# Kernel tuning notes

Hardware: AMD Instinct MI355X
Metric: run time of the kernel (lower is better)

The kernel has to match this reference:

```python
import jax, jax.numpy as jnp
import numpy as np

N_NODES = 100000
N_EDGES = 1600000
IN_DIM = 256
HID_DIM = 128


def gcn_conv(x, W, b, row, col, norm, n_nodes):
    """PyG-style GCNConv: out[col] += norm * (x @ W)[row], then + bias.

    row/col/norm already include self-loops and symmetric normalization.
    """
    xw = x @ W                                  # [N, D_out]
    msgs = xw[row] * norm[:, None]              # [E', D_out]
    out = jax.ops.segment_sum(msgs, col, num_segments=n_nodes)
    return out + b


def _build_norm(edge_index, n_nodes):
    # add self-loops
    loops = jnp.arange(n_nodes, dtype=edge_index.dtype)
    row = jnp.concatenate([edge_index[0], loops])
    col = jnp.concatenate([edge_index[1], loops])
    # symmetric normalization: deg computed over target (col), as in PyG gcn_norm
    deg = jax.ops.segment_sum(jnp.ones_like(col, dtype=jnp.float32), col,
                              num_segments=n_nodes)
    dinv = jnp.where(deg > 0, jax.lax.rsqrt(deg), 0.0)
    norm = dinv[row] * dinv[col]
    return row, col, norm


def setup_inputs() -> dict:
    key = jax.random.key(0)
    k1, k2, k3, k4 = jax.random.split(key, 4)
    x = jax.random.normal(k1, (N_NODES, IN_DIM), dtype=jnp.float32)
    edge_index = jax.random.randint(k2, (2, N_EDGES), 0, N_NODES, dtype=jnp.int64)
    # Glorot-ish init for weights
    W1 = jax.random.normal(k3, (IN_DIM, HID_DIM), dtype=jnp.float32) / np.sqrt(IN_DIM)
    W2 = jax.random.normal(k4, (HID_DIM, HID_DIM), dtype=jnp.float32) / np.sqrt(HID_DIM)
    b1 = jnp.zeros((HID_DIM,), dtype=jnp.float32)
    b2 = jnp.zeros((HID_DIM,), dtype=jnp.float32)
    return {"x": x, "edge_index": edge_index, "W1": W1, "b1": b1, "W2": W2, "b2": b2}


def reference(x, edge_index, W1, b1, W2, b2):
    n_nodes = x.shape[0]
    row, col, norm = _build_norm(edge_index, n_nodes)
    h = jnp.tanh(gcn_conv(x, W1, b1, row, col, norm, n_nodes))
    h = jnp.tanh(gcn_conv(h, W2, b2, row, col, norm, n_nodes))
    return h
```

## Files before the change

kernel.cpp:

```cpp
#include <hip/hip_runtime.h>
#include <cstdint>
#include <cstddef>

#define N_NODES 100000
#define N_EDGES 1600000
#define HID 128
#define SCAN_BLOCKS ((N_NODES + 255) / 256)

using frag_ab = __attribute__((ext_vector_type(8))) short;
using f32x4   = __attribute__((ext_vector_type(4))) float;

__device__ __forceinline__ unsigned short f2bf(float f) {
    uint32_t u = __builtin_bit_cast(uint32_t, f);
    u += 0x7fffu + ((u >> 16) & 1u);
    return (unsigned short)(u >> 16);
}
__device__ __forceinline__ float bf2f(unsigned short u) {
    uint32_t v = (uint32_t)u << 16;
    return __builtin_bit_cast(float, v);
}

__global__ __launch_bounds__(256) void k_count(const int* __restrict__ col,
                                               int* __restrict__ deg) {
    int e = blockIdx.x * 256 + threadIdx.x;
    if (e < N_EDGES) atomicAdd(&deg[col[e]], 1);
}

__global__ __launch_bounds__(256) void k_dinv(const int* __restrict__ deg,
                                              float* __restrict__ dinv) {
    int i = blockIdx.x * 256 + threadIdx.x;
    if (i < N_NODES) dinv[i] = rsqrtf((float)deg[i] + 1.0f);
}

__global__ __launch_bounds__(256) void k_scan1(const int* __restrict__ deg,
                                               int* __restrict__ cursor,
                                               int* __restrict__ bsum) {
    __shared__ int s[256];
    const int t = threadIdx.x;
    const int i = blockIdx.x * 256 + t;
    int v = (i < N_NODES) ? deg[i] : 0;
    s[t] = v;
    __syncthreads();
#pragma unroll
    for (int d = 1; d < 256; d <<= 1) {
        int a = (t >= d) ? s[t - d] : 0;
        __syncthreads();
        s[t] += a;
        __syncthreads();
    }
    if (i < N_NODES) cursor[i] = s[t] - v;
    if (t == 255) bsum[blockIdx.x] = s[t];
}

__global__ __launch_bounds__(512) void k_scan2(int* __restrict__ bsum, int n) {
    __shared__ int s[512];
    const int t = threadIdx.x;
    int v = (t < n) ? bsum[t] : 0;
    s[t] = v;
    __syncthreads();
#pragma unroll
    for (int d = 1; d < 512; d <<= 1) {
        int a = (t >= d) ? s[t - d] : 0;
        __syncthreads();
        s[t] += a;
        __syncthreads();
    }
    if (t < n) bsum[t] = s[t] - v;
}

__global__ __launch_bounds__(256) void k_scan3(int* __restrict__ cursor,
                                               const int* __restrict__ bsum) {
    const int i = blockIdx.x * 256 + threadIdx.x;
    if (i < N_NODES) cursor[i] += bsum[blockIdx.x];
}

__global__ __launch_bounds__(256) void k_place(const int* __restrict__ row,
                                               const int* __restrict__ col,
                                               const float* __restrict__ dinv,
                                               int* __restrict__ cursor,
                                               int* __restrict__ srow,
                                               float* __restrict__ sdnv) {
    const int e = blockIdx.x * 256 + threadIdx.x;
    if (e >= N_EDGES) return;
    const int r = row[e];
    const int c = col[e];
    const int p = atomicAdd(&cursor[c], 1);
    srow[p] = r;
    sdnv[p] = dinv[r];
}

template <int K>
__global__ __launch_bounds__(256) void k_wt(const float* __restrict__ W,
                                            short* __restrict__ Wt) {
    const int idx = blockIdx.x * 256 + threadIdx.x;
    if (idx >= K * HID) return;
    const int k = idx >> 7;
    const int n = idx & 127;
    Wt[n * K + k] = (short)f2bf(W[idx]);
}

template <int K>
__global__ __launch_bounds__(256) void k_mfma_f32A(const float* __restrict__ A,
                                                   const short* __restrict__ Wt,
                                                   unsigned short* __restrict__ C) {
    const int tid  = threadIdx.x;
    const int w    = tid >> 6;
    const int lane = tid & 63;
    const int l15  = lane & 15;
    const int kg   = lane >> 4;
    const int m0   = blockIdx.x * 128;

    f32x4 acc[2][8];
#pragma unroll
    for (int rb = 0; rb < 2; ++rb)
#pragma unroll
        for (int c = 0; c < 8; ++c)
            acc[rb][c] = (f32x4){0.f, 0.f, 0.f, 0.f};

    for (int k0 = 0; k0 < K; k0 += 32) {
        frag_ab afr[2];
#pragma unroll
        for (int rb = 0; rb < 2; ++rb) {
            int ar = m0 + w * 16 + rb * 64 + l15;
            if (ar >= N_NODES) ar = N_NODES - 1;
            const float4* ap =
                reinterpret_cast<const float4*>(A + (size_t)ar * K + k0 + kg * 8);
            const float4 v0 = ap[0];
            const float4 v1 = ap[1];
            afr[rb][0] = (short)f2bf(v0.x); afr[rb][1] = (short)f2bf(v0.y);
            afr[rb][2] = (short)f2bf(v0.z); afr[rb][3] = (short)f2bf(v0.w);
            afr[rb][4] = (short)f2bf(v1.x); afr[rb][5] = (short)f2bf(v1.y);
            afr[rb][6] = (short)f2bf(v1.z); afr[rb][7] = (short)f2bf(v1.w);
        }
#pragma unroll
        for (int c = 0; c < 8; ++c) {
            const frag_ab bfr = *reinterpret_cast<const frag_ab*>(
                Wt + (size_t)(c * 16 + l15) * K + k0 + kg * 8);
            acc[0][c] = __builtin_amdgcn_mfma_f32_16x16x32_bf16(afr[0], bfr, acc[0][c], 0, 0, 0);
            acc[1][c] = __builtin_amdgcn_mfma_f32_16x16x32_bf16(afr[1], bfr, acc[1][c], 0, 0, 0);
        }
    }
#pragma unroll
    for (int rb = 0; rb < 2; ++rb) {
        const int rbase = m0 + w * 16 + rb * 64 + kg * 4;
#pragma unroll
        for (int c = 0; c < 8; ++c)
#pragma unroll
            for (int i = 0; i < 4; ++i) {
                const int rr = rbase + i;
                if (rr < N_NODES) C[(size_t)rr * HID + c * 16 + l15] = f2bf(acc[rb][c][i]);
            }
    }
}

template <int K>
__global__ __launch_bounds__(256) void k_mfma_bf16A(const unsigned short* __restrict__ A,
                                                    const short* __restrict__ Wt,
                                                    unsigned short* __restrict__ C) {
    const int tid  = threadIdx.x;
    const int w    = tid >> 6;
    const int lane = tid & 63;
    const int l15  = lane & 15;
    const int kg   = lane >> 4;
    const int m0   = blockIdx.x * 128;

    f32x4 acc[2][8];
#pragma unroll
    for (int rb = 0; rb < 2; ++rb)
#pragma unroll
        for (int c = 0; c < 8; ++c)
            acc[rb][c] = (f32x4){0.f, 0.f, 0.f, 0.f};

    for (int k0 = 0; k0 < K; k0 += 32) {
        frag_ab afr[2];
#pragma unroll
        for (int rb = 0; rb < 2; ++rb) {
            int ar = m0 + w * 16 + rb * 64 + l15;
            if (ar >= N_NODES) ar = N_NODES - 1;
            afr[rb] = *reinterpret_cast<const frag_ab*>(A + (size_t)ar * K + k0 + kg * 8);
        }
#pragma unroll
        for (int c = 0; c < 8; ++c) {
            const frag_ab bfr = *reinterpret_cast<const frag_ab*>(
                Wt + (size_t)(c * 16 + l15) * K + k0 + kg * 8);
            acc[0][c] = __builtin_amdgcn_mfma_f32_16x16x32_bf16(afr[0], bfr, acc[0][c], 0, 0, 0);
            acc[1][c] = __builtin_amdgcn_mfma_f32_16x16x32_bf16(afr[1], bfr, acc[1][c], 0, 0, 0);
        }
    }
#pragma unroll
    for (int rb = 0; rb < 2; ++rb) {
        const int rbase = m0 + w * 16 + rb * 64 + kg * 4;
#pragma unroll
        for (int c = 0; c < 8; ++c)
#pragma unroll
            for (int i = 0; i < 4; ++i) {
                const int rr = rbase + i;
                if (rr < N_NODES) C[(size_t)rr * HID + c * 16 + l15] = f2bf(acc[rb][c][i]);
            }
    }
}

template <bool OUT_BF16>
__global__ __launch_bounds__(256) void k_gather_act(const unsigned short* __restrict__ xw,
                                                    const int* __restrict__ srow,
                                                    const float* __restrict__ sdnv,
                                                    const int* __restrict__ cursor,
                                                    const float* __restrict__ dinv,
                                                    const float* __restrict__ b,
                                                    void* __restrict__ outv) {
    const int tid = threadIdx.x;
    const int node = blockIdx.x * 8 + (tid >> 5);
    if (node >= N_NODES) return;
    const int ch = (tid & 31) * 4;

    const int start = (node == 0) ? 0 : cursor[node - 1];
    const int end = cursor[node];

    float4 acc = make_float4(0.f, 0.f, 0.f, 0.f);
#pragma unroll 2
    for (int j = start; j < end; ++j) {
        const int r = srow[j];
        const float w = sdnv[j];
        const ushort4 v = *reinterpret_cast<const ushort4*>(xw + (size_t)r * HID + ch);
        acc.x += w * bf2f(v.x);
        acc.y += w * bf2f(v.y);
        acc.z += w * bf2f(v.z);
        acc.w += w * bf2f(v.w);
    }

    const float dc = dinv[node];
    const float s = dc * dc;
    const ushort4 xv = *reinterpret_cast<const ushort4*>(xw + (size_t)node * HID + ch);
    const float4 bv = *reinterpret_cast<const float4*>(b + ch);
    float o0 = tanhf(dc * acc.x + s * bf2f(xv.x) + bv.x);
    float o1 = tanhf(dc * acc.y + s * bf2f(xv.y) + bv.y);
    float o2 = tanhf(dc * acc.z + s * bf2f(xv.z) + bv.z);
    float o3 = tanhf(dc * acc.w + s * bf2f(xv.w) + bv.w);

    if (OUT_BF16) {
        ushort4 o = {f2bf(o0), f2bf(o1), f2bf(o2), f2bf(o3)};
        *reinterpret_cast<ushort4*>((unsigned short*)outv + (size_t)node * HID + ch) = o;
    } else {
        *reinterpret_cast<float4*>((float*)outv + (size_t)node * HID + ch) =
            make_float4(o0, o1, o2, o3);
    }
}

extern "C" void kernel_launch(void* const* d_in, const int* in_sizes, int n_in,
                              void* d_out, int out_size, void* d_ws, size_t ws_size,
                              hipStream_t stream) {
    const float* x  = (const float*)d_in[0];
    const int*   ei = (const int*)d_in[1];
    const int*   row = ei;
    const int*   col = ei + N_EDGES;
    const float* W1 = (const float*)d_in[2];
    const float* b1 = (const float*)d_in[3];
    const float* W2 = (const float*)d_in[4];
    const float* b2 = (const float*)d_in[5];
    float* out = (float*)d_out;

    unsigned short* xwb = (unsigned short*)d_ws;
    unsigned short* h1b = xwb + (size_t)N_NODES * HID;
    float* dinv   = (float*)(h1b + (size_t)N_NODES * HID);
    int*   deg    = (int*)(dinv + N_NODES);
    int*   cursor = deg + N_NODES;
    int*   bsum   = cursor + N_NODES;
    int*   srow   = bsum + 512;
    float* sdnv   = (float*)(srow + N_EDGES);
    short* wt1    = (short*)(sdnv + N_EDGES);
    short* wt2    = wt1 + 128 * 256;

    k_wt<256><<<(256 * HID + 255) / 256, 256, 0, stream>>>(W1, wt1);
    k_wt<128><<<(128 * HID + 255) / 256, 256, 0, stream>>>(W2, wt2);

    hipMemsetAsync(deg, 0, N_NODES * sizeof(int), stream);
    k_count<<<(N_EDGES + 255) / 256, 256, 0, stream>>>(col, deg);
    k_dinv<<<(N_NODES + 255) / 256, 256, 0, stream>>>(deg, dinv);
    k_scan1<<<SCAN_BLOCKS, 256, 0, stream>>>(deg, cursor, bsum);
    k_scan2<<<1, 512, 0, stream>>>(bsum, SCAN_BLOCKS);
    k_scan3<<<SCAN_BLOCKS, 256, 0, stream>>>(cursor, bsum);
    k_place<<<(N_EDGES + 255) / 256, 256, 0, stream>>>(row, col, dinv, cursor, srow, sdnv);

    k_mfma_f32A<256><<<(N_NODES + 127) / 128, 256, 0, stream>>>(x, wt1, xwb);
    k_gather_act<true><<<N_NODES / 8, 256, 0, stream>>>(xwb, srow, sdnv, cursor, dinv, b1, h1b);

    k_mfma_bf16A<128><<<(N_NODES + 127) / 128, 256, 0, stream>>>(h1b, wt2, xwb);
    k_gather_act<false><<<N_NODES / 8, 256, 0, stream>>>(xwb, srow, sdnv, cursor, dinv, b2, out);
}
```

Baseline: 558.3 us.

## Fold source-node dinv scaling into GEMM epilogue and drop per-edge weight array

```diff
diff --git a/kernel.cpp b/kernel.cpp
--- a/kernel.cpp
+++ b/kernel.cpp
@@ -76,17 +76,14 @@
 
 __global__ __launch_bounds__(256) void k_place(const int* __restrict__ row,
                                                const int* __restrict__ col,
-                                               const float* __restrict__ dinv,
                                                int* __restrict__ cursor,
-                                               int* __restrict__ srow,
-                                               float* __restrict__ sdnv) {
+                                               int* __restrict__ srow) {
     const int e = blockIdx.x * 256 + threadIdx.x;
     if (e >= N_EDGES) return;
     const int r = row[e];
     const int c = col[e];
     const int p = atomicAdd(&cursor[c], 1);
     srow[p] = r;
-    sdnv[p] = dinv[r];
 }
 
 template <int K>
@@ -102,6 +99,7 @@
 template <int K>
 __global__ __launch_bounds__(256) void k_mfma_f32A(const float* __restrict__ A,
                                                    const short* __restrict__ Wt,
+                                                   const float* __restrict__ dinv,
                                                    unsigned short* __restrict__ C) {
     const int tid  = threadIdx.x;
     const int w    = tid >> 6;
@@ -143,12 +141,17 @@
 #pragma unroll
     for (int rb = 0; rb < 2; ++rb) {
         const int rbase = m0 + w * 16 + rb * 64 + kg * 4;
+        float dv[4];
+#pragma unroll
+        for (int i = 0; i < 4; ++i)
+            dv[i] = (rbase + i < N_NODES) ? dinv[rbase + i] : 0.f;
 #pragma unroll
         for (int c = 0; c < 8; ++c)
 #pragma unroll
             for (int i = 0; i < 4; ++i) {
                 const int rr = rbase + i;
-                if (rr < N_NODES) C[(size_t)rr * HID + c * 16 + l15] = f2bf(acc[rb][c][i]);
+                if (rr < N_NODES)
+                    C[(size_t)rr * HID + c * 16 + l15] = f2bf(dv[i] * acc[rb][c][i]);
             }
     }
 }
@@ -156,6 +159,7 @@
 template <int K>
 __global__ __launch_bounds__(256) void k_mfma_bf16A(const unsigned short* __restrict__ A,
                                                     const short* __restrict__ Wt,
+                                                    const float* __restrict__ dinv,
                                                     unsigned short* __restrict__ C) {
     const int tid  = threadIdx.x;
     const int w    = tid >> 6;
@@ -190,20 +194,24 @@
 #pragma unroll
     for (int rb = 0; rb < 2; ++rb) {
         const int rbase = m0 + w * 16 + rb * 64 + kg * 4;
+        float dv[4];
+#pragma unroll
+        for (int i = 0; i < 4; ++i)
+            dv[i] = (rbase + i < N_NODES) ? dinv[rbase + i] : 0.f;
 #pragma unroll
         for (int c = 0; c < 8; ++c)
 #pragma unroll
             for (int i = 0; i < 4; ++i) {
                 const int rr = rbase + i;
-                if (rr < N_NODES) C[(size_t)rr * HID + c * 16 + l15] = f2bf(acc[rb][c][i]);
+                if (rr < N_NODES)
+                    C[(size_t)rr * HID + c * 16 + l15] = f2bf(dv[i] * acc[rb][c][i]);
             }
     }
 }
 
 template <bool OUT_BF16>
-__global__ __launch_bounds__(256) void k_gather_act(const unsigned short* __restrict__ xw,
+__global__ __launch_bounds__(256) void k_gather_act(const unsigned short* __restrict__ xws,
                                                     const int* __restrict__ srow,
-                                                    const float* __restrict__ sdnv,
                                                     const int* __restrict__ cursor,
                                                     const float* __restrict__ dinv,
                                                     const float* __restrict__ b,
@@ -220,22 +228,20 @@
 #pragma unroll 2
     for (int j = start; j < end; ++j) {
         const int r = srow[j];
-        const float w = sdnv[j];
-        const ushort4 v = *reinterpret_cast<const ushort4*>(xw + (size_t)r * HID + ch);
-        acc.x += w * bf2f(v.x);
-        acc.y += w * bf2f(v.y);
-        acc.z += w * bf2f(v.z);
-        acc.w += w * bf2f(v.w);
+        const ushort4 v = *reinterpret_cast<const ushort4*>(xws + (size_t)r * HID + ch);
+        acc.x += bf2f(v.x);
+        acc.y += bf2f(v.y);
+        acc.z += bf2f(v.z);
+        acc.w += bf2f(v.w);
     }
 
     const float dc = dinv[node];
-    const float s = dc * dc;
-    const ushort4 xv = *reinterpret_cast<const ushort4*>(xw + (size_t)node * HID + ch);
+    const ushort4 xv = *reinterpret_cast<const ushort4*>(xws + (size_t)node * HID + ch);
     const float4 bv = *reinterpret_cast<const float4*>(b + ch);
-    float o0 = tanhf(dc * acc.x + s * bf2f(xv.x) + bv.x);
-    float o1 = tanhf(dc * acc.y + s * bf2f(xv.y) + bv.y);
-    float o2 = tanhf(dc * acc.z + s * bf2f(xv.z) + bv.z);
-    float o3 = tanhf(dc * acc.w + s * bf2f(xv.w) + bv.w);
+    float o0 = tanhf(dc * (acc.x + bf2f(xv.x)) + bv.x);
+    float o1 = tanhf(dc * (acc.y + bf2f(xv.y)) + bv.y);
+    float o2 = tanhf(dc * (acc.z + bf2f(xv.z)) + bv.z);
+    float o3 = tanhf(dc * (acc.w + bf2f(xv.w)) + bv.w);
 
     if (OUT_BF16) {
         ushort4 o = {f2bf(o0), f2bf(o1), f2bf(o2), f2bf(o3)};
@@ -266,8 +272,7 @@
     int*   cursor = deg + N_NODES;
     int*   bsum   = cursor + N_NODES;
     int*   srow   = bsum + 512;
-    float* sdnv   = (float*)(srow + N_EDGES);
-    short* wt1    = (short*)(sdnv + N_EDGES);
+    short* wt1    = (short*)(srow + N_EDGES);
     short* wt2    = wt1 + 128 * 256;
 
     k_wt<256><<<(256 * HID + 255) / 256, 256, 0, stream>>>(W1, wt1);
@@ -279,11 +284,11 @@
     k_scan1<<<SCAN_BLOCKS, 256, 0, stream>>>(deg, cursor, bsum);
     k_scan2<<<1, 512, 0, stream>>>(bsum, SCAN_BLOCKS);
     k_scan3<<<SCAN_BLOCKS, 256, 0, stream>>>(cursor, bsum);
-    k_place<<<(N_EDGES + 255) / 256, 256, 0, stream>>>(row, col, dinv, cursor, srow, sdnv);
-
-    k_mfma_f32A<256><<<(N_NODES + 127) / 128, 256, 0, stream>>>(x, wt1, xwb);
-    k_gather_act<true><<<N_NODES / 8, 256, 0, stream>>>(xwb, srow, sdnv, cursor, dinv, b1, h1b);
-
-    k_mfma_bf16A<128><<<(N_NODES + 127) / 128, 256, 0, stream>>>(h1b, wt2, xwb);
-    k_gather_act<false><<<N_NODES / 8, 256, 0, stream>>>(xwb, srow, sdnv, cursor, dinv, b2, out);
-}
+    k_place<<<(N_EDGES + 255) / 256, 256, 0, stream>>>(row, col, cursor, srow);
+
+    k_mfma_f32A<256><<<(N_NODES + 127) / 128, 256, 0, stream>>>(x, wt1, dinv, xwb);
+    k_gather_act<true><<<N_NODES / 8, 256, 0, stream>>>(xwb, srow, cursor, dinv, b1, h1b);
+
+    k_mfma_bf16A<128><<<(N_NODES + 127) / 128, 256, 0, stream>>>(h1b, wt2, dinv, xwb);
+    k_gather_act<false><<<N_NODES / 8, 256, 0, stream>>>(xwb, srow, cursor, dinv, b2, out);
+}
```

New measurement: 588.3 us. +5.4%, slower.
